# Kernel optimization log

Measured on AMD Instinct MI355X. Metric: run time of the kernel, lower is better.

## Reference

```python
import jax, jax.numpy as jnp
import numpy as np

NOISE_DB = 40.0  # layer's `noise` ctor arg (SNR in dB)


def setup_inputs() -> dict:
    key = jax.random.key(0)
    k1, k2, k3 = jax.random.split(key, 3)
    B, M, L, S = 4, 256, 24, 22  # S = shots = round(M*L/(M+L-1))
    x = jax.random.normal(k1, (B, M, M, L), dtype=jnp.float32)
    # coded aperture weights, init N(0,1)/sqrt(kern*kern) as in build()
    H = jax.random.normal(k2, (1, M, M, 1, S), dtype=jnp.float32) / np.float32(M)
    # standard-normal noise sample (the layer draws this internally)
    noise_eps = jax.random.normal(k3, (B, M, M + L - 1, 1), dtype=jnp.float32)
    return {"x": x, "H": H, "noise_eps": noise_eps}


def reference(x, H, noise_eps):
    B, M, _, L = x.shape
    S = H.shape[-1]
    W = M + L - 1  # dispersed detector width
    H2 = H[0, :, :, 0, :]  # (M, M, S)

    # Aux1 = H * x : (B, M, M, L, S)
    HX = H2[None, :, :, None, :] * x[..., None]

    # Forward shear-sum: Y[b,m,n,s] = sum_i HX[b,m,n-i,i,s]
    # (equivalent to the pad + L rolls + extract-band-i + reduce_sum)
    Y = jnp.zeros((B, M, W, S), dtype=x.dtype)
    for i in range(L):  # fixed small spectral loop; indexed accumulation, no padded rolls
        Y = Y.at[:, :, i:i + M, :].add(HX[:, :, :, i, :])

    # Noise: sigma^2 = ||Y||^2 / (M * W * B * 10^(noise/10)); broadcast over shots
    sigm = jnp.sum(Y * Y) / (M * W * B * (10.0 ** (NOISE_DB / 10.0)))
    Y = Y + jnp.sqrt(sigm) * noise_eps  # noise_eps: (B, M, W, 1)

    # Reverse shift-extract: X[b,m,n,i] = sum_s H2[m,n,s] * Y[b,m,n+i,s]
    Ys = jnp.stack([Y[:, :, i:i + M, :] for i in range(L)], axis=3)  # (B,M,M,L,S)
    X = jnp.einsum('bmnls,mns->bmnl', Ys, H2)

    return X / jnp.max(X)
```

## Files before the change

kernel.cpp:

```cpp
#include <hip/hip_runtime.h>
#include <math.h>

namespace {
constexpr int Mz = 256, Lz = 24, Sz = 22, Bz = 4;
constexpr int Wz = Mz + Lz - 1;
constexpr int ST = 26;
constexpr int NBLK = Bz * Mz;
constexpr int NPASS = 7;
constexpr double SIGM_DEN = (double)Mz * (double)Wz * (double)Bz * 1e4;
}

__device__ __forceinline__ unsigned int enc_f32(float f) {
  unsigned int u = __float_as_uint(f);
  return (u & 0x80000000u) ? ~u : (u | 0x80000000u);
}
__device__ __forceinline__ float dec_f32(unsigned int e) {
  unsigned int u = (e & 0x80000000u) ? (e ^ 0x80000000u) : ~e;
  return __uint_as_float(u);
}

__device__ __forceinline__ float rot_down1(float v) {
  return __int_as_float(
      __builtin_amdgcn_update_dpp(0, __float_as_int(v), 0x130, 0xF, 0xF, true));
}

__global__ __launch_bounds__(256, 4) void k_fwd(const float* __restrict__ x,
                                                const float* __restrict__ H,
                                                float* __restrict__ X0,
                                                double* __restrict__ sumsq,
                                                float* __restrict__ hsum)
{
  __shared__ __align__(16) float Ys[Wz * ST];
  __shared__ double wred[4];

  const int tid = threadIdx.x;
  const int j  = tid & 63;
  const int wv = tid >> 6;
  const int b = blockIdx.x >> 8;
  const int m = blockIdx.x & 255;
  const float* __restrict__ xp = x + (size_t)(b * Mz + m) * (Mz * Lz);
  const float* __restrict__ Hp = H + (size_t)m * (Mz * Sz);

  double local = 0.0;

  for (int pp = 0; pp < 2; ++pp) {
    const int p = wv + 4 * pp;
    if (p >= NPASS) break;
    const int W0 = 41 * p;
    const int n = W0 - 23 + j;
    const bool valid = (n >= 0) && (n < Mz);

    float hr[Sz], xr[Lz];
    if (valid) {
      const float2* __restrict__ h2 = (const float2*)(Hp + n * Sz);
      #pragma unroll
      for (int k = 0; k < 11; ++k) { const float2 h = h2[k]; hr[2*k] = h.x; hr[2*k+1] = h.y; }
      const float4* __restrict__ x4 = (const float4*)(xp + n * Lz);
      #pragma unroll
      for (int k = 0; k < 6; ++k) {
        const float4 t = x4[k];
        xr[4*k] = t.x; xr[4*k+1] = t.y; xr[4*k+2] = t.z; xr[4*k+3] = t.w;
      }
    } else {
      #pragma unroll
      for (int k = 0; k < Sz; ++k) hr[k] = 0.f;
      #pragma unroll
      for (int k = 0; k < Lz; ++k) xr[k] = 0.f;
    }

    float acc[Sz];
    #pragma unroll
    for (int s = 0; s < Sz; ++s) acc[s] = 0.f;

    #pragma unroll
    for (int i = 0; i < Lz; ++i) {
      #pragma unroll
      for (int s = 0; s < Sz; ++s) acc[s] = fmaf(hr[s], xr[i], acc[s]);
      if (i < Lz - 1) {
        #pragma unroll
        for (int s = 0; s < Sz; ++s) acc[s] = rot_down1(acc[s]);
      }
    }

    const int w = W0 + j;
    if (j <= 40 && w < Wz) {
      float2* __restrict__ yrow = (float2*)&Ys[w * ST];
      #pragma unroll
      for (int k = 0; k < 11; ++k) {
        yrow[k] = make_float2(acc[2*k], acc[2*k+1]);
        local += (double)acc[2*k] * acc[2*k] + (double)acc[2*k+1] * acc[2*k+1];
      }
    }
  }

  for (int off = 32; off > 0; off >>= 1) local += __shfl_down(local, off, 64);
  const int lane = tid & 63, wid = tid >> 6;
  if (lane == 0) wred[wid] = local;
  __syncthreads();
  if (tid == 0) atomicAdd(sumsq, wred[0] + wred[1] + wred[2] + wred[3]);

  {
    const int n = tid;
    float hr[Sz];
    {
      const float2* __restrict__ h2 = (const float2*)(Hp + n * Sz);
      #pragma unroll
      for (int k = 0; k < 11; ++k) { const float2 h = h2[k]; hr[2*k] = h.x; hr[2*k+1] = h.y; }
    }
    if (b == 0) {
      float a = 0.f;
      #pragma unroll
      for (int s = 0; s < Sz; ++s) a += hr[s];
      hsum[(m << 8) + n] = a;
    }
    float4* __restrict__ Xp4 =
        (float4*)(X0 + (size_t)(b * Mz + m) * (Mz * Lz) + n * Lz);
    #pragma unroll
    for (int q = 0; q < 6; ++q) {
      float o[4];
      #pragma unroll
      for (int jj = 0; jj < 4; ++jj) {
        const int l = 4 * q + jj;
        const float2* __restrict__ yr = (const float2*)&Ys[(n + l) * ST];
        float a0 = 0.f, a1 = 0.f;
        #pragma unroll
        for (int k = 0; k < 11; ++k) {
          const float2 y = yr[k];
          a0 = fmaf(y.x, hr[2*k],   a0);
          a1 = fmaf(y.y, hr[2*k+1], a1);
        }
        o[jj] = a0 + a1;
      }
      Xp4[q] = make_float4(o[0], o[1], o[2], o[3]);
    }
  }
}

__global__ __launch_bounds__(256) void k_max(const float* __restrict__ X0,
                                             const float* __restrict__ eps,
                                             const float* __restrict__ hsum,
                                             const double* __restrict__ sumsq,
                                             unsigned int* __restrict__ maxenc)
{
  const float c = sqrtf((float)(*sumsq / SIGM_DEN));
  const int tid = threadIdx.x;
  const int bm = blockIdx.x;
  const int m = bm & 255;
  const float4* __restrict__ slab = (const float4*)(X0 + (size_t)bm * (Mz * Lz));
  const float* __restrict__ ep = eps + bm * Wz;
  const float* __restrict__ hs = hsum + (m << 8);

  float mx = -3.4e38f;
  #pragma unroll
  for (int q = 0; q < 6; ++q) {
    const int idx4 = q * 256 + tid;
    const int n = idx4 / 6;
    const int l0 = 4 * (idx4 - 6 * n);
    const float4 t = slab[idx4];
    const float hv = c * hs[n];
    const float* __restrict__ e4 = ep + n + l0;
    mx = fmaxf(mx, fmaf(hv, e4[0], t.x));
    mx = fmaxf(mx, fmaf(hv, e4[1], t.y));
    mx = fmaxf(mx, fmaf(hv, e4[2], t.z));
    mx = fmaxf(mx, fmaf(hv, e4[3], t.w));
  }
  for (int off = 32; off > 0; off >>= 1) mx = fmaxf(mx, __shfl_down(mx, off, 64));
  __shared__ float wredf[4];
  const int lane = tid & 63, wid = tid >> 6;
  if (lane == 0) wredf[wid] = mx;
  __syncthreads();
  if (tid == 0) {
    float bmx = fmaxf(fmaxf(wredf[0], wredf[1]), fmaxf(wredf[2], wredf[3]));
    atomicMax(maxenc, enc_f32(bmx));
  }
}

__global__ __launch_bounds__(256) void k_final(float* __restrict__ Xio,
                                               const float* __restrict__ eps,
                                               const float* __restrict__ hsum,
                                               const double* __restrict__ sumsq,
                                               const unsigned int* __restrict__ maxenc)
{
  const float c = sqrtf((float)(*sumsq / SIGM_DEN));
  const float inv = 1.0f / dec_f32(*maxenc);
  const int tid = threadIdx.x;
  const int bm = blockIdx.x;
  const int m = bm & 255;
  float4* __restrict__ slab = (float4*)(Xio + (size_t)bm * (Mz * Lz));
  const float* __restrict__ ep = eps + bm * Wz;
  const float* __restrict__ hs = hsum + (m << 8);

  #pragma unroll
  for (int q = 0; q < 6; ++q) {
    const int idx4 = q * 256 + tid;
    const int n = idx4 / 6;
    const int l0 = 4 * (idx4 - 6 * n);
    float4 t = slab[idx4];
    const float hv = c * hs[n];
    const float* __restrict__ e4 = ep + n + l0;
    t.x = fmaf(hv, e4[0], t.x) * inv;
    t.y = fmaf(hv, e4[1], t.y) * inv;
    t.z = fmaf(hv, e4[2], t.z) * inv;
    t.w = fmaf(hv, e4[3], t.w) * inv;
    slab[idx4] = t;
  }
}

extern "C" void kernel_launch(void* const* d_in, const int* in_sizes, int n_in,
                              void* d_out, int out_size, void* d_ws, size_t ws_size,
                              hipStream_t stream) {
  const float* x   = (const float*)d_in[0];
  const float* H   = (const float*)d_in[1];
  const float* eps = (const float*)d_in[2];
  float* out = (float*)d_out;

  double*       sumsq  = (double*)d_ws;
  unsigned int* maxenc = (unsigned int*)((char*)d_ws + 8);
  float*        hsum   = (float*)((char*)d_ws + 16);

  hipMemsetAsync(d_ws, 0, 16, stream);
  k_fwd   <<<NBLK, 256, 0, stream>>>(x, H, out, sumsq, hsum);
  k_max   <<<NBLK, 256, 0, stream>>>(out, eps, hsum, sumsq, maxenc);
  k_final <<<NBLK, 256, 0, stream>>>(out, eps, hsum, sumsq, maxenc);
}
```

Measured before the change: 124.3 us.

## Fuse forward, max and normalize into one cooperative kernel with grid syncs

Replaces the three-kernel pipeline with a single cooperative kernel that keeps each block's unnormalized X slab in registers across two grid-wide barriers: one after the sum-of-squares reduction and one after the global max. This is meant to remove the round trips of the intermediate X0 through global memory and the extra kernel launches. The output is staged through shared memory so global stores stay coalesced. It requires all 1024 blocks to be co-resident, which depends on 4 blocks per CU with the enlarged LDS footprint. If the cooperative launch fails it falls back to the old three kernels.

```diff
diff --git a/kernel.cpp b/kernel.cpp
--- a/kernel.cpp
+++ b/kernel.cpp
@@ -1,5 +1,8 @@
 #include <hip/hip_runtime.h>
+#include <hip/hip_cooperative_groups.h>
 #include <math.h>
+
+namespace cg = cooperative_groups;
 
 namespace {
 constexpr int Mz = 256, Lz = 24, Sz = 22, Bz = 4;
@@ -24,6 +27,158 @@
       __builtin_amdgcn_update_dpp(0, __float_as_int(v), 0x130, 0xF, 0xF, true));
 }
 
+template <typename YSTORE>
+__device__ __forceinline__ double y_build(const float* __restrict__ xp,
+                                          const float* __restrict__ Hp,
+                                          int j, int wv, YSTORE&& store)
+{
+  double local = 0.0;
+  for (int pp = 0; pp < 2; ++pp) {
+    const int p = wv + 4 * pp;
+    if (p >= NPASS) break;
+    const int W0 = 41 * p;
+    const int n = W0 - 23 + j;
+    const bool valid = (n >= 0) && (n < Mz);
+
+    float hr[Sz], xr[Lz];
+    if (valid) {
+      const float2* __restrict__ h2 = (const float2*)(Hp + n * Sz);
+      #pragma unroll
+      for (int k = 0; k < 11; ++k) { const float2 h = h2[k]; hr[2*k] = h.x; hr[2*k+1] = h.y; }
+      const float4* __restrict__ x4 = (const float4*)(xp + n * Lz);
+      #pragma unroll
+      for (int k = 0; k < 6; ++k) {
+        const float4 t = x4[k];
+        xr[4*k] = t.x; xr[4*k+1] = t.y; xr[4*k+2] = t.z; xr[4*k+3] = t.w;
+      }
+    } else {
+      #pragma unroll
+      for (int k = 0; k < Sz; ++k) hr[k] = 0.f;
+      #pragma unroll
+      for (int k = 0; k < Lz; ++k) xr[k] = 0.f;
+    }
+
+    float acc[Sz];
+    #pragma unroll
+    for (int s = 0; s < Sz; ++s) acc[s] = 0.f;
+
+    #pragma unroll
+    for (int i = 0; i < Lz; ++i) {
+      #pragma unroll
+      for (int s = 0; s < Sz; ++s) acc[s] = fmaf(hr[s], xr[i], acc[s]);
+      if (i < Lz - 1) {
+        #pragma unroll
+        for (int s = 0; s < Sz; ++s) acc[s] = rot_down1(acc[s]);
+      }
+    }
+
+    const int w = W0 + j;
+    if (j <= 40 && w < Wz) {
+      store(w, acc);
+      #pragma unroll
+      for (int s = 0; s < Sz; ++s) local += (double)acc[s] * acc[s];
+    }
+  }
+  return local;
+}
+
+__global__ __launch_bounds__(256, 4) void k_fused(const float* __restrict__ x,
+                                                  const float* __restrict__ H,
+                                                  const float* __restrict__ eps,
+                                                  float* __restrict__ out,
+                                                  double* __restrict__ sumsq,
+                                                  unsigned int* __restrict__ maxenc)
+{
+  __shared__ __align__(16) float Ys[Wz * ST];
+  __shared__ float eps_s[Wz];
+  __shared__ double wred[4];
+  __shared__ float wredf[4];
+
+  const int tid = threadIdx.x;
+  const int j  = tid & 63;
+  const int wv = tid >> 6;
+  const int bm = blockIdx.x;
+  const int m = bm & 255;
+  const float* __restrict__ xp = x + (size_t)bm * (Mz * Lz);
+  const float* __restrict__ Hp = H + (size_t)m * (Mz * Sz);
+
+  for (int e = tid; e < Wz; e += 256) eps_s[e] = eps[bm * Wz + e];
+
+  double local = y_build(xp, Hp, j, wv, [&](int w, const float* acc) {
+    float2* __restrict__ yrow = (float2*)&Ys[w * ST];
+    #pragma unroll
+    for (int k = 0; k < 11; ++k) yrow[k] = make_float2(acc[2*k], acc[2*k+1]);
+  });
+
+  for (int off = 32; off > 0; off >>= 1) local += __shfl_down(local, off, 64);
+  if ((tid & 63) == 0) wred[wv] = local;
+  __syncthreads();
+  if (tid == 0) atomicAdd(sumsq, wred[0] + wred[1] + wred[2] + wred[3]);
+
+  float X0r[Lz];
+  float hsumloc;
+  {
+    const int n = tid;
+    float hr[Sz];
+    const float2* __restrict__ h2 = (const float2*)(Hp + n * Sz);
+    #pragma unroll
+    for (int k = 0; k < 11; ++k) { const float2 h = h2[k]; hr[2*k] = h.x; hr[2*k+1] = h.y; }
+    float a = 0.f;
+    #pragma unroll
+    for (int s = 0; s < Sz; ++s) a += hr[s];
+    hsumloc = a;
+    #pragma unroll
+    for (int l = 0; l < Lz; ++l) {
+      const float2* __restrict__ yr = (const float2*)&Ys[(n + l) * ST];
+      float a0 = 0.f, a1 = 0.f;
+      #pragma unroll
+      for (int k = 0; k < 11; ++k) {
+        const float2 y = yr[k];
+        a0 = fmaf(y.x, hr[2*k],   a0);
+        a1 = fmaf(y.y, hr[2*k+1], a1);
+      }
+      X0r[l] = a0 + a1;
+    }
+  }
+
+  cg::this_grid().sync();
+
+  const double ss = __hip_atomic_load(sumsq, __ATOMIC_ACQUIRE, __HIP_MEMORY_SCOPE_AGENT);
+  const float c = sqrtf((float)(ss / SIGM_DEN));
+  const float hv = c * hsumloc;
+  float mx = -3.4e38f;
+  #pragma unroll
+  for (int l = 0; l < Lz; ++l) {
+    X0r[l] = fmaf(hv, eps_s[tid + l], X0r[l]);
+    mx = fmaxf(mx, X0r[l]);
+  }
+  for (int off = 32; off > 0; off >>= 1) mx = fmaxf(mx, __shfl_down(mx, off, 64));
+  if ((tid & 63) == 0) wredf[wv] = mx;
+  __syncthreads();
+  if (tid == 0) {
+    float bmx = fmaxf(fmaxf(wredf[0], wredf[1]), fmaxf(wredf[2], wredf[3]));
+    atomicMax(maxenc, enc_f32(bmx));
+  }
+
+  cg::this_grid().sync();
+
+  const unsigned int me = __hip_atomic_load(maxenc, __ATOMIC_ACQUIRE, __HIP_MEMORY_SCOPE_AGENT);
+  const float inv = 1.0f / dec_f32(me);
+  float* __restrict__ Xl = Ys;
+  #pragma unroll
+  for (int l = 0; l < Lz; ++l) Xl[tid * 25 + l] = X0r[l] * inv;
+  __syncthreads();
+  float4* __restrict__ op4 = (float4*)(out + (size_t)bm * (Mz * Lz));
+  #pragma unroll
+  for (int q = 0; q < 6; ++q) {
+    const int idx4 = q * 256 + tid;
+    const int n = idx4 / 6;
+    const int l0 = 4 * (idx4 - 6 * n);
+    const float* __restrict__ src = &Xl[n * 25 + l0];
+    op4[idx4] = make_float4(src[0], src[1], src[2], src[3]);
+  }
+}
+
 __global__ __launch_bounds__(256, 4) void k_fwd(const float* __restrict__ x,
                                                 const float* __restrict__ H,
                                                 float* __restrict__ X0,
@@ -41,72 +196,23 @@
   const float* __restrict__ xp = x + (size_t)(b * Mz + m) * (Mz * Lz);
   const float* __restrict__ Hp = H + (size_t)m * (Mz * Sz);
 
-  double local = 0.0;
-
-  for (int pp = 0; pp < 2; ++pp) {
-    const int p = wv + 4 * pp;
-    if (p >= NPASS) break;
-    const int W0 = 41 * p;
-    const int n = W0 - 23 + j;
-    const bool valid = (n >= 0) && (n < Mz);
-
-    float hr[Sz], xr[Lz];
-    if (valid) {
-      const float2* __restrict__ h2 = (const float2*)(Hp + n * Sz);
-      #pragma unroll
-      for (int k = 0; k < 11; ++k) { const float2 h = h2[k]; hr[2*k] = h.x; hr[2*k+1] = h.y; }
-      const float4* __restrict__ x4 = (const float4*)(xp + n * Lz);
-      #pragma unroll
-      for (int k = 0; k < 6; ++k) {
-        const float4 t = x4[k];
-        xr[4*k] = t.x; xr[4*k+1] = t.y; xr[4*k+2] = t.z; xr[4*k+3] = t.w;
-      }
-    } else {
-      #pragma unroll
-      for (int k = 0; k < Sz; ++k) hr[k] = 0.f;
-      #pragma unroll
-      for (int k = 0; k < Lz; ++k) xr[k] = 0.f;
-    }
-
-    float acc[Sz];
-    #pragma unroll
-    for (int s = 0; s < Sz; ++s) acc[s] = 0.f;
-
-    #pragma unroll
-    for (int i = 0; i < Lz; ++i) {
-      #pragma unroll
-      for (int s = 0; s < Sz; ++s) acc[s] = fmaf(hr[s], xr[i], acc[s]);
-      if (i < Lz - 1) {
-        #pragma unroll
-        for (int s = 0; s < Sz; ++s) acc[s] = rot_down1(acc[s]);
-      }
-    }
-
-    const int w = W0 + j;
-    if (j <= 40 && w < Wz) {
-      float2* __restrict__ yrow = (float2*)&Ys[w * ST];
-      #pragma unroll
-      for (int k = 0; k < 11; ++k) {
-        yrow[k] = make_float2(acc[2*k], acc[2*k+1]);
-        local += (double)acc[2*k] * acc[2*k] + (double)acc[2*k+1] * acc[2*k+1];
-      }
-    }
-  }
+  double local = y_build(xp, Hp, j, wv, [&](int w, const float* acc) {
+    float2* __restrict__ yrow = (float2*)&Ys[w * ST];
+    #pragma unroll
+    for (int k = 0; k < 11; ++k) yrow[k] = make_float2(acc[2*k], acc[2*k+1]);
+  });
 
   for (int off = 32; off > 0; off >>= 1) local += __shfl_down(local, off, 64);
-  const int lane = tid & 63, wid = tid >> 6;
-  if (lane == 0) wred[wid] = local;
+  if ((tid & 63) == 0) wred[wv] = local;
   __syncthreads();
   if (tid == 0) atomicAdd(sumsq, wred[0] + wred[1] + wred[2] + wred[3]);
 
   {
     const int n = tid;
     float hr[Sz];
-    {
-      const float2* __restrict__ h2 = (const float2*)(Hp + n * Sz);
-      #pragma unroll
-      for (int k = 0; k < 11; ++k) { const float2 h = h2[k]; hr[2*k] = h.x; hr[2*k+1] = h.y; }
-    }
+    const float2* __restrict__ h2 = (const float2*)(Hp + n * Sz);
+    #pragma unroll
+    for (int k = 0; k < 11; ++k) { const float2 h = h2[k]; hr[2*k] = h.x; hr[2*k+1] = h.y; }
     if (b == 0) {
       float a = 0.f;
       #pragma unroll
@@ -219,7 +325,14 @@
   float*        hsum   = (float*)((char*)d_ws + 16);
 
   hipMemsetAsync(d_ws, 0, 16, stream);
-  k_fwd   <<<NBLK, 256, 0, stream>>>(x, H, out, sumsq, hsum);
-  k_max   <<<NBLK, 256, 0, stream>>>(out, eps, hsum, sumsq, maxenc);
-  k_final <<<NBLK, 256, 0, stream>>>(out, eps, hsum, sumsq, maxenc);
-}
+
+  void* args[] = { (void*)&x, (void*)&H, (void*)&eps, (void*)&out,
+                   (void*)&sumsq, (void*)&maxenc };
+  hipError_t err = hipLaunchCooperativeKernel((void*)k_fused, dim3(NBLK), dim3(256),
+                                              args, 0, stream);
+  if (err != hipSuccess) {
+    k_fwd   <<<NBLK, 256, 0, stream>>>(x, H, out, sumsq, hsum);
+    k_max   <<<NBLK, 256, 0, stream>>>(out, eps, hsum, sumsq, maxenc);
+    k_final <<<NBLK, 256, 0, stream>>>(out, eps, hsum, sumsq, maxenc);
+  }
+}
```

New measurement: 380.4 us. +206.1%, slower.
